# Kernel optimization log

Hardware: AMD Instinct MI355X
Metric: run time of the kernel (lower is better)

## Reference

```python
import jax, jax.numpy as jnp
import numpy as np

EXP_ORDER = 2  # matches init_kwargs exp_order
N_FEAT = 8
Q_DIM = 1
BATCH = 262144
T_EXPANDED = 164  # n + C(n+1,2) + C(n+2,3) for n=8, degrees 1..3
N_OUT = 8


def taylor_expand(x, exp_order):
    """Faithful vectorized version of the nested multiply/concat loop.

    x: [B, n, q]. Builds all monomials of degree 1..exp_order+1 using the same
    recursion as the TF code: at each order, for each j, multiply x_j with the
    previous-order block starting at Id[j], then append. The q-loop in the
    original is replaced by broadcasting over the q axis (identical math).
    """
    n = x.shape[1]
    Id = list(range(n))  # start index of x_j's block in the previous-order terms
    epd = x
    for _ in range(exp_order):
        L = epd.shape[1]  # slice end Id[n-1]+1 always equals current length
        blocks = []
        new_Id = []
        offset = L
        for j in range(n):
            blk = x[:, j:j + 1, :] * epd[:, Id[j]:L, :]  # [B, L-Id[j], q]
            new_Id.append(offset)
            offset += blk.shape[1]
            blocks.append(blk)
        epd = jnp.concatenate([epd] + blocks, axis=1)
        Id = new_Id
    return epd


def setup_inputs() -> dict:
    key = jax.random.key(0)
    k1, k2, k3 = jax.random.split(key, 3)
    x = jax.random.normal(k1, (BATCH, N_FEAT, Q_DIM), dtype=jnp.float32)
    # 'dl' init: uniform(-1/sqrt(fan), 1/sqrt(fan)) with fan = weights_shape[0]
    dl_scale = 1.0 / np.sqrt(N_OUT)
    W = jax.random.uniform(k2, (N_OUT, T_EXPANDED), minval=-dl_scale,
                           maxval=dl_scale, dtype=jnp.float32)
    # 'uniform' bias init: U(-0.2, 0.2), shape [out, 1]
    b = jax.random.uniform(k3, (N_OUT, 1), minval=-0.2, maxval=0.2,
                           dtype=jnp.float32)
    return {"x": x, "W": W, "b": b}


def reference(x, W, b):
    # cp_type == 'none': pass-through of the input
    epd = taylor_expand(x, EXP_ORDER)          # [B, T, q]
    out = jnp.einsum('ot,btq->boq', W, epd) + b[None]  # [B, out, q]
    # act_type == 'relu'
    return jax.nn.relu(out)
```

## Files before the change

kernel.cpp:

```cpp
#include <hip/hip_runtime.h>


static constexpr int NOUT = 8;
static constexpr int TEXP = 164;

__device__ __forceinline__ float relu(float v) { return fmaxf(v, 0.0f); }

__global__ __launch_bounds__(256) void taylor_kernel(
    const float* __restrict__ x, const float* __restrict__ W,
    const float* __restrict__ b, float* __restrict__ out, int n) {
  int i = blockIdx.x * blockDim.x + threadIdx.x;
  if (i >= n) return;

  float4 xa = reinterpret_cast<const float4*>(x)[i * 2 + 0];
  float4 xb = reinterpret_cast<const float4*>(x)[i * 2 + 1];
  float xv[8] = {xa.x, xa.y, xa.z, xa.w, xb.x, xb.y, xb.z, xb.w};

  float acc[NOUT];
#pragma unroll
  for (int o = 0; o < NOUT; ++o) acc[o] = b[o];

  int t = 0;

#pragma unroll
  for (int j = 0; j < 8; ++j) {
    float m = xv[j];
#pragma unroll
    for (int o = 0; o < NOUT; ++o) acc[o] = fmaf(W[o * TEXP + t], m, acc[o]);
    ++t;
  }

  float d2[36];
  int p = 0;
#pragma unroll
  for (int j = 0; j < 8; ++j) {
#pragma unroll
    for (int k = j; k < 8; ++k) {
      float m = xv[j] * xv[k];
      d2[p] = m;
      ++p;
#pragma unroll
      for (int o = 0; o < NOUT; ++o) acc[o] = fmaf(W[o * TEXP + t], m, acc[o]);
      ++t;
    }
  }

#pragma unroll
  for (int j = 0; j < 8; ++j) {
#pragma unroll
    for (int a = j; a < 8; ++a) {
      int rowstart = a * 8 - a * (a - 1) / 2 - a;
#pragma unroll
      for (int bb = a; bb < 8; ++bb) {
        float m = xv[j] * d2[rowstart + bb];
#pragma unroll
        for (int o = 0; o < NOUT; ++o) acc[o] = fmaf(W[o * TEXP + t], m, acc[o]);
        ++t;
      }
    }
  }

  float4 o0 = make_float4(relu(acc[0]), relu(acc[1]), relu(acc[2]), relu(acc[3]));
  float4 o1 = make_float4(relu(acc[4]), relu(acc[5]), relu(acc[6]), relu(acc[7]));
  reinterpret_cast<float4*>(out)[i * 2 + 0] = o0;
  reinterpret_cast<float4*>(out)[i * 2 + 1] = o1;
}

extern "C" void kernel_launch(void* const* d_in, const int* in_sizes, int n_in,
                              void* d_out, int out_size, void* d_ws, size_t ws_size,
                              hipStream_t stream) {
  const float* x = (const float*)d_in[0];
  const float* W = (const float*)d_in[1];
  const float* b = (const float*)d_in[2];
  float* out = (float*)d_out;

  int n = in_sizes[0] / 8;
  int block = 256;
  int grid = (n + block - 1) / block;
  taylor_kernel<<<grid, block, 0, stream>>>(x, W, b, out, n);
}
```

Before: 19.92 us.

## Compute Taylor-expanded linear layer with bf16 MFMA and a persistent grid

New measurement: 17.64 us. -11.4%, faster.

```diff
diff --git a/kernel.cpp b/kernel.cpp
--- a/kernel.cpp
+++ b/kernel.cpp
@@ -1,69 +1,154 @@
 #include <hip/hip_runtime.h>
+#include <hip/hip_bf16.h>
+#include <string.h>
 
 
+static constexpr int TEXP = 164;
 static constexpr int NOUT = 8;
-static constexpr int TEXP = 164;
+static constexpr int NMFMA = 11;
+static constexpr int HALF = 88;
 
-__device__ __forceinline__ float relu(float v) { return fmaxf(v, 0.0f); }
+using f32x16 = __attribute__((ext_vector_type(16))) float;
+using short8 = __attribute__((ext_vector_type(8))) short;
 
-__global__ __launch_bounds__(256) void taylor_kernel(
-    const float* __restrict__ x, const float* __restrict__ W,
-    const float* __restrict__ b, float* __restrict__ out, int n) {
-  int i = blockIdx.x * blockDim.x + threadIdx.x;
-  if (i >= n) return;
+constexpr int rowstart2(int j) { return j * 8 - j * (j - 1) / 2; }
+constexpr int start3(int j) {
+  int s = 44;
+  for (int jp = 0; jp < j; ++jp) s += (8 - jp) * (9 - jp) / 2;
+  return s;
+}
+struct D3 { int j, p; };
+constexpr D3 d3idx(int M) {
+  int j = 0;
+  while (start3(j + 1) <= M) ++j;
+  int q = M - start3(j);
+  int a = j;
+  while (q >= (8 - a)) { q -= (8 - a); ++a; }
+  int b = a + q;
+  return { j, rowstart2(a) + (b - a) };
+}
 
-  float4 xa = reinterpret_cast<const float4*>(x)[i * 2 + 0];
-  float4 xb = reinterpret_cast<const float4*>(x)[i * 2 + 1];
-  float xv[8] = {xa.x, xa.y, xa.z, xa.w, xb.x, xb.y, xb.z, xb.w};
+template <int M>
+__device__ __forceinline__ float mono(const float (&xv)[8], const float (&d2)[36]) {
+  if constexpr (M < 8) {
+    return xv[M];
+  } else if constexpr (M < 44) {
+    return d2[M - 8];
+  } else {
+    constexpr D3 t = d3idx(M);
+    return xv[t.j] * d2[t.p];
+  }
+}
 
-  float acc[NOUT];
+__device__ __forceinline__ short bf16bits(float v) {
+  __hip_bfloat16 h = __float2bfloat16(v);
+  short s;
+  memcpy(&s, &h, 2);
+  return s;
+}
+
+template <int C>
+__device__ __forceinline__ void do_slot(const float (&xv)[8], const float (&d2)[36],
+                                        bool hi, short8& bv) {
+  float v0 = mono<C>(xv, d2);
+  float v1;
+  if constexpr (HALF + C < TEXP) v1 = mono<HALF + C>(xv, d2);
+  else v1 = 0.0f;
+  float v = hi ? v1 : v0;
+  bv[C & 7] = bf16bits(v);
+}
+
+template <int I>
+__device__ __forceinline__ void slot8(const float (&xv)[8], const float (&d2)[36],
+                                      bool hi, short8& bv) {
+  do_slot<8 * I + 0>(xv, d2, hi, bv);
+  do_slot<8 * I + 1>(xv, d2, hi, bv);
+  do_slot<8 * I + 2>(xv, d2, hi, bv);
+  do_slot<8 * I + 3>(xv, d2, hi, bv);
+  do_slot<8 * I + 4>(xv, d2, hi, bv);
+  do_slot<8 * I + 5>(xv, d2, hi, bv);
+  do_slot<8 * I + 6>(xv, d2, hi, bv);
+  do_slot<8 * I + 7>(xv, d2, hi, bv);
+}
+
+template <int I>
+struct MfmaStep {
+  static __device__ __forceinline__ void run(const float (&xv)[8], const float (&d2)[36],
+                                             bool hi, const short8 (&af)[NMFMA],
+                                             f32x16& acc) {
+    short8 bv;
+    slot8<I>(xv, d2, hi, bv);
+    acc = __builtin_amdgcn_mfma_f32_32x32x16_bf16(af[I], bv, acc, 0, 0, 0);
+    MfmaStep<I + 1>::run(xv, d2, hi, af, acc);
+  }
+};
+template <>
+struct MfmaStep<NMFMA> {
+  static __device__ __forceinline__ void run(const float (&)[8], const float (&)[36],
+                                             bool, const short8 (&)[NMFMA], f32x16&) {}
+};
+
+__global__ void prep_w(const float* __restrict__ W, unsigned short* __restrict__ wp) {
+  for (int idx = threadIdx.x + blockIdx.x * blockDim.x; idx < NMFMA * 64 * 8;
+       idx += blockDim.x * gridDim.x) {
+    int j = idx & 7;
+    int lane = (idx >> 3) & 63;
+    int i = idx >> 9;
+    int row = lane & 31, h = lane >> 5;
+    int m = HALF * h + 8 * i + j;
+    float v = (row < NOUT && m < TEXP) ? W[row * TEXP + m] : 0.0f;
+    union { float f; unsigned int u; } c; c.f = v;
+    unsigned int u = c.u;
+    wp[idx] = (unsigned short)((u + 0x7fffu + ((u >> 16) & 1u)) >> 16);
+  }
+}
+
+__global__ __launch_bounds__(256) void taylor_mfma(
+    const float* __restrict__ x, const float* __restrict__ b,
+    const unsigned short* __restrict__ wp, float* __restrict__ out, int ngroups) {
+  const int lane = (int)(threadIdx.x & 63);
+  const bool hi = lane >= 32;
+  const int col = lane & 31;
+  const int h4 = hi ? 4 : 0;
+
+  short8 afrag[NMFMA];
 #pragma unroll
-  for (int o = 0; o < NOUT; ++o) acc[o] = b[o];
+  for (int i = 0; i < NMFMA; ++i)
+    afrag[i] = *reinterpret_cast<const short8*>(wp + (i * 64 + lane) * 8);
 
-  int t = 0;
+  const float4 bv4 = *reinterpret_cast<const float4*>(b + h4);
 
+  const int wave = (int)((blockIdx.x * blockDim.x + threadIdx.x) >> 6);
+  const int nw = (int)((gridDim.x * blockDim.x) >> 6);
+
+  for (int g = wave; g < ngroups; g += nw) {
+    const int elem = g * 32 + col;
+    float4 xa = reinterpret_cast<const float4*>(x)[elem * 2 + 0];
+    float4 xb = reinterpret_cast<const float4*>(x)[elem * 2 + 1];
+    float xv[8] = {xa.x, xa.y, xa.z, xa.w, xb.x, xb.y, xb.z, xb.w};
+
+    float d2[36];
 #pragma unroll
-  for (int j = 0; j < 8; ++j) {
-    float m = xv[j];
+    for (int j = 0; j < 8; ++j) {
 #pragma unroll
-    for (int o = 0; o < NOUT; ++o) acc[o] = fmaf(W[o * TEXP + t], m, acc[o]);
-    ++t;
-  }
-
-  float d2[36];
-  int p = 0;
-#pragma unroll
-  for (int j = 0; j < 8; ++j) {
-#pragma unroll
-    for (int k = j; k < 8; ++k) {
-      float m = xv[j] * xv[k];
-      d2[p] = m;
-      ++p;
-#pragma unroll
-      for (int o = 0; o < NOUT; ++o) acc[o] = fmaf(W[o * TEXP + t], m, acc[o]);
-      ++t;
-    }
-  }
-
-#pragma unroll
-  for (int j = 0; j < 8; ++j) {
-#pragma unroll
-    for (int a = j; a < 8; ++a) {
-      int rowstart = a * 8 - a * (a - 1) / 2 - a;
-#pragma unroll
-      for (int bb = a; bb < 8; ++bb) {
-        float m = xv[j] * d2[rowstart + bb];
-#pragma unroll
-        for (int o = 0; o < NOUT; ++o) acc[o] = fmaf(W[o * TEXP + t], m, acc[o]);
-        ++t;
+      for (int k = j; k < 8; ++k) {
+        d2[rowstart2(j) + (k - j)] = xv[j] * xv[k];
       }
     }
+
+    f32x16 acc;
+#pragma unroll
+    for (int r = 0; r < 16; ++r) acc[r] = 0.0f;
+
+    MfmaStep<0>::run(xv, d2, hi, afrag, acc);
+
+    float4 o;
+    o.x = fmaxf(acc[0] + bv4.x, 0.0f);
+    o.y = fmaxf(acc[1] + bv4.y, 0.0f);
+    o.z = fmaxf(acc[2] + bv4.z, 0.0f);
+    o.w = fmaxf(acc[3] + bv4.w, 0.0f);
+    reinterpret_cast<float4*>(out)[elem * 2 + (hi ? 1 : 0)] = o;
   }
-
-  float4 o0 = make_float4(relu(acc[0]), relu(acc[1]), relu(acc[2]), relu(acc[3]));
-  float4 o1 = make_float4(relu(acc[4]), relu(acc[5]), relu(acc[6]), relu(acc[7]));
-  reinterpret_cast<float4*>(out)[i * 2 + 0] = o0;
-  reinterpret_cast<float4*>(out)[i * 2 + 1] = o1;
 }
 
 extern "C" void kernel_launch(void* const* d_in, const int* in_sizes, int n_in,
@@ -73,9 +158,11 @@
   const float* W = (const float*)d_in[1];
   const float* b = (const float*)d_in[2];
   float* out = (float*)d_out;
+  unsigned short* wp = (unsigned short*)d_ws;
 
   int n = in_sizes[0] / 8;
-  int block = 256;
-  int grid = (n + block - 1) / block;
-  taylor_kernel<<<grid, block, 0, stream>>>(x, W, b, out, n);
+  int ngroups = n / 32;
+
+  prep_w<<<8, 256, 0, stream>>>(W, wp);
+  taylor_mfma<<<1024, 256, 0, stream>>>(x, b, wp, out, ngroups);
 }
```
